# Performance work log

Measured on AMD Instinct MI355X. Metric: run time of the kernel, lower is better.

## Reference

```python
import jax, jax.numpy as jnp
import numpy as np

N = 100000        # nodes
E = 1600000       # edges (avg degree 16)
IN_C = 128
HID = 128
OUT_C = 18


def setup_inputs() -> dict:
    key = jax.random.key(0)
    k_x, k_e, k_w1, k_b1, k_w2, k_b2 = jax.random.split(key, 6)
    x = jax.random.normal(k_x, (N, IN_C), dtype=jnp.float32)
    edge_index = jax.random.randint(k_e, (2, E), 0, N, dtype=jnp.int64)
    # Glorot-ish init for linear weights, zero bias (PyG GCNConv defaults)
    W1 = jax.random.normal(k_w1, (IN_C, HID), dtype=jnp.float32) / np.sqrt(IN_C)
    b1 = jnp.zeros((HID,), dtype=jnp.float32)
    W2 = jax.random.normal(k_w2, (HID, OUT_C), dtype=jnp.float32) / np.sqrt(HID)
    b2 = jnp.zeros((OUT_C,), dtype=jnp.float32)
    return {"x": x, "edge_index": edge_index, "W1": W1, "b1": b1, "W2": W2, "b2": b2}


def _gcn_conv(x, src, dst, norm, W, b, n_nodes):
    # PyG GCNConv: linear transform, then normalized scatter-add aggregation
    h = x @ W                                   # [N, d_out]
    msg = h[src] * norm[:, None]                # gather + scale: [E+N, d_out]
    out = jax.ops.segment_sum(msg, dst, num_segments=n_nodes)
    return out + b


def reference(x, edge_index, W1, b1, W2, b2):
    src, dst = edge_index[0], edge_index[1]
    loop = jnp.arange(N, dtype=edge_index.dtype)
    src_f = jnp.concatenate([src, loop])        # add self-loops
    dst_f = jnp.concatenate([dst, loop])
    # symmetric normalization deg^-1/2[src] * deg^-1/2[dst] (with self-loops)
    deg = jax.ops.segment_sum(jnp.ones_like(dst_f, dtype=x.dtype), dst_f, num_segments=N)
    dinv = jnp.where(deg > 0, jax.lax.rsqrt(deg), 0.0)
    norm = dinv[src_f] * dinv[dst_f]            # [E+N]

    h = _gcn_conv(x, src_f, dst_f, norm, W1, b1, N)
    h = jax.nn.relu(h)
    # dropout is identity in eval mode (training=False)
    h = _gcn_conv(h, src_f, dst_f, norm, W2, b2, N)
    return jax.nn.log_softmax(h, axis=1)
```

## Files before the change

kernel.cpp:

```cpp
#include <hip/hip_runtime.h>
#include <math.h>

#define NN 100000
#define NE 1600000
#define CH  128
#define CO  18
#define NPB 256
#define NBUK ((NN + NPB - 1) / NPB)
#define EPB 4096
#define NBB ((NE + EPB - 1) / EPB)

typedef unsigned int uint;
typedef unsigned short ushort;
typedef float floatx4 __attribute__((ext_vector_type(4)));
typedef short short8 __attribute__((ext_vector_type(8)));
typedef ushort ushort4v __attribute__((ext_vector_type(4)));

__device__ __forceinline__ float bf_lo(uint u) { return __uint_as_float(u << 16); }
__device__ __forceinline__ float bf_hi(uint u) { return __uint_as_float(u & 0xFFFF0000u); }
__device__ __forceinline__ ushort f2bf(float f) {
    uint u = __float_as_uint(f);
    u += 0x7FFFu + ((u >> 16) & 1u);
    return (ushort)(u >> 16);
}
__device__ __forceinline__ uint pack_bf16(float a, float b) {
    return (uint)f2bf(a) | ((uint)f2bf(b) << 16);
}


union FatLDS {
    int h[NBUK];
    struct { ushort As[128 * 128]; ushort Bs[128 * 128]; } g;
};

__global__ __launch_bounds__(256, 2) void k_fat1(const int* __restrict__ dst,
                                                 int* __restrict__ bcnt,
                                                 const float* __restrict__ x,
                                                 const float* __restrict__ W1,
                                                 ushort* __restrict__ h1s) {
    __shared__ FatLDS L;
    int tid = threadIdx.x;

    if (blockIdx.x < NBB) {
        for (int i = tid; i < NBUK; i += 256) L.h[i] = 0;
        __syncthreads();
        int e0 = blockIdx.x * EPB;
#pragma unroll
        for (int i = 0; i < EPB / 256; ++i) {
            int e = e0 + i * 256 + tid;
            if (e < NE) atomicAdd(&L.h[dst[e] >> 8], 1);
        }
        __syncthreads();
        for (int i = tid; i < NBUK; i += 256)
            if (L.h[i]) atomicAdd(&bcnt[i], L.h[i]);
        return;
    }

    int row0 = (blockIdx.x - NBB) * 128;

    for (int p = tid; p < 8192; p += 256) {
        int kp = p >> 7, n = p & 127;
        float w0 = W1[(2 * kp) * 128 + n];
        float w1 = W1[(2 * kp + 1) * 128 + n];
        ((uint*)L.g.Bs)[(n * 64 + kp) ^ ((n & 7) << 2)] = pack_bf16(w0, w1);
    }
    for (int i = 0; i < 16; ++i) {
        int flat = i * 256 + tid;
        int r = flat >> 5, c4 = flat & 31;
        int gr = row0 + r;
        float4 v = (gr < NN) ? ((const float4*)x)[(size_t)gr * 32 + c4]
                             : make_float4(0.f, 0.f, 0.f, 0.f);
        ushort4v p;
        p.x = f2bf(v.x); p.y = f2bf(v.y); p.z = f2bf(v.z); p.w = f2bf(v.w);
        int idx = (r * 128 + c4 * 4) ^ ((r & 7) << 3);
        *(ushort4v*)&L.g.As[idx] = p;
    }
    __syncthreads();

    int lane = tid & 63;
    int wave = tid >> 6;
    int wrow = wave * 32;
    int lr = lane & 15;
    int lk8 = (lane >> 4) * 8;

    floatx4 acc[2][8];
#pragma unroll
    for (int a = 0; a < 2; ++a)
#pragma unroll
        for (int b = 0; b < 8; ++b) acc[a][b] = (floatx4)(0.0f);

#pragma unroll
    for (int ks = 0; ks < 4; ++ks) {
        int k0 = ks * 32 + lk8;
        int r0r = wrow + lr;
        int r1r = wrow + 16 + lr;
        short8 a0 = *(const short8*)&L.g.As[(r0r * 128 + k0) ^ ((r0r & 7) << 3)];
        short8 a1 = *(const short8*)&L.g.As[(r1r * 128 + k0) ^ ((r1r & 7) << 3)];
#pragma unroll
        for (int nt = 0; nt < 8; ++nt) {
            int n = nt * 16 + lr;
            short8 bf = *(const short8*)&L.g.Bs[(n * 128 + k0) ^ ((n & 7) << 3)];
            acc[0][nt] = __builtin_amdgcn_mfma_f32_16x16x32_bf16(a0, bf, acc[0][nt], 0, 0, 0);
            acc[1][nt] = __builtin_amdgcn_mfma_f32_16x16x32_bf16(a1, bf, acc[1][nt], 0, 0, 0);
        }
    }

    int drow = (lane >> 4) * 4;
#pragma unroll
    for (int rt = 0; rt < 2; ++rt) {
#pragma unroll
        for (int i = 0; i < 4; ++i) {
            int gr = row0 + wrow + rt * 16 + drow + i;
            if (gr < NN) {
                size_t base = (size_t)gr * 128;
#pragma unroll
                for (int nt = 0; nt < 8; ++nt)
                    h1s[base + nt * 16 + lr] = f2bf(acc[rt][nt][i]);
            }
        }
    }
}


__global__ __launch_bounds__(512) void k_bscan(const int* __restrict__ bcnt,
                                               int* __restrict__ bbase,
                                               int* __restrict__ bcur) {
    __shared__ int s[512];
    int tid = threadIdx.x;
    int c = (tid < NBUK) ? bcnt[tid] : 0;
    s[tid] = c;
    __syncthreads();
    for (int off = 1; off < 512; off <<= 1) {
        int t = (tid >= off) ? s[tid - off] : 0;
        __syncthreads();
        s[tid] += t;
        __syncthreads();
    }
    if (tid < NBUK) {
        int ex = s[tid] - c;
        bbase[tid] = ex;
        bcur[tid] = ex;
    }
    if (tid == NBUK) bbase[NBUK] = NE;
}

__global__ __launch_bounds__(256) void k_bin(const int* __restrict__ src,
                                             const int* __restrict__ dst,
                                             int* __restrict__ bcur,
                                             uint* __restrict__ etmp) {
    __shared__ int h[NBUK];
    __shared__ int base[NBUK];
    int tid = threadIdx.x;
    for (int i = tid; i < NBUK; i += 256) h[i] = 0;
    __syncthreads();

    int e0 = blockIdx.x * EPB;
    int sv[EPB / 256], dv[EPB / 256];
#pragma unroll
    for (int i = 0; i < EPB / 256; ++i) {
        int e = e0 + i * 256 + tid;
        if (e < NE) {
            sv[i] = src[e];
            dv[i] = dst[e];
            atomicAdd(&h[dv[i] >> 8], 1);
        } else {
            dv[i] = -1;
        }
    }
    __syncthreads();
    for (int i = tid; i < NBUK; i += 256)
        base[i] = h[i] ? atomicAdd(&bcur[i], h[i]) : 0;
    __syncthreads();
    for (int i = tid; i < NBUK; i += 256) h[i] = 0;
    __syncthreads();
#pragma unroll
    for (int i = 0; i < EPB / 256; ++i) {
        if (dv[i] >= 0) {
            int b = dv[i] >> 8;
            int pos = base[b] + atomicAdd(&h[b], 1);
            etmp[pos] = ((uint)sv[i] << 8) | ((uint)dv[i] & 255u);
        }
    }
}

__global__ __launch_bounds__(256) void k_pass2(const int* __restrict__ bbase,
                                               const uint* __restrict__ etmp,
                                               int* __restrict__ row_start,
                                               float* __restrict__ dinv,
                                               int* __restrict__ csr_src) {
    __shared__ int hist[NPB];
    __shared__ int s[NPB];
    __shared__ int cur[NPB];
    int tid = threadIdx.x;
    int b = blockIdx.x;
    int e0 = bbase[b], e1 = bbase[b + 1];

    hist[tid] = 0;
    __syncthreads();
    for (int e = e0 + tid; e < e1; e += 256)
        atomicAdd(&hist[etmp[e] & 255u], 1);
    __syncthreads();

    int c = hist[tid];
    s[tid] = c;
    __syncthreads();
    for (int off = 1; off < 256; off <<= 1) {
        int t = (tid >= off) ? s[tid - off] : 0;
        __syncthreads();
        s[tid] += t;
        __syncthreads();
    }
    int pfx = s[tid] - c;
    s[tid] = pfx;
    cur[tid] = 0;

    int node = b * NPB + tid;
    if (node < NN) {
        row_start[node] = e0 + pfx;
        dinv[node] = rsqrtf((float)c + 1.0f);
    }
    if (b == NBUK - 1 && tid == 0) row_start[NN] = NE;
    __syncthreads();

    for (int e = e0 + tid; e < e1; e += 256) {
        uint r = etmp[e];
        int n = (int)(r & 255u);
        int p = e0 + s[n] + atomicAdd(&cur[n], 1);
        csr_src[p] = (int)(r >> 8);
    }
}


__global__ __launch_bounds__(256) void k_agg1(const int* __restrict__ row_start,
                                              const int* __restrict__ csr_src,
                                              const float* __restrict__ dinv,
                                              const uint* __restrict__ h1u,
                                              const float* __restrict__ b1,
                                              uint* __restrict__ h1ru) {
    int wave = threadIdx.x >> 6;
    int lane = threadIdx.x & 63;
    int i = blockIdx.x * 4 + wave;
    if (i >= NN) return;
    int r0 = row_start[i], r1 = row_start[i + 1];
    float di = dinv[i];
    float ax = 0.0f, ay = 0.0f;

    int j = r0;
    for (; j + 7 < r1; j += 8) {
        int s0 = csr_src[j],     s1 = csr_src[j + 1];
        int s2 = csr_src[j + 2], s3 = csr_src[j + 3];
        int s4 = csr_src[j + 4], s5 = csr_src[j + 5];
        int s6 = csr_src[j + 6], s7 = csr_src[j + 7];
        float w0 = dinv[s0] * di, w1 = dinv[s1] * di;
        float w2 = dinv[s2] * di, w3 = dinv[s3] * di;
        float w4 = dinv[s4] * di, w5 = dinv[s5] * di;
        float w6 = dinv[s6] * di, w7 = dinv[s7] * di;
        uint u0 = h1u[(size_t)s0 * 64 + lane];
        uint u1 = h1u[(size_t)s1 * 64 + lane];
        uint u2 = h1u[(size_t)s2 * 64 + lane];
        uint u3 = h1u[(size_t)s3 * 64 + lane];
        uint u4 = h1u[(size_t)s4 * 64 + lane];
        uint u5 = h1u[(size_t)s5 * 64 + lane];
        uint u6 = h1u[(size_t)s6 * 64 + lane];
        uint u7 = h1u[(size_t)s7 * 64 + lane];
        ax += w0 * bf_lo(u0) + w1 * bf_lo(u1) + w2 * bf_lo(u2) + w3 * bf_lo(u3)
            + w4 * bf_lo(u4) + w5 * bf_lo(u5) + w6 * bf_lo(u6) + w7 * bf_lo(u7);
        ay += w0 * bf_hi(u0) + w1 * bf_hi(u1) + w2 * bf_hi(u2) + w3 * bf_hi(u3)
            + w4 * bf_hi(u4) + w5 * bf_hi(u5) + w6 * bf_hi(u6) + w7 * bf_hi(u7);
    }
    for (; j < r1; ++j) {
        int s0 = csr_src[j];
        float w0 = dinv[s0] * di;
        uint u0 = h1u[(size_t)s0 * 64 + lane];
        ax += w0 * bf_lo(u0);
        ay += w0 * bf_hi(u0);
    }

    uint us = h1u[(size_t)i * 64 + lane];
    float2 bb = ((const float2*)b1)[lane];
    float di2 = di * di;
    float ox = fmaxf(ax + di2 * bf_lo(us) + bb.x, 0.0f);
    float oy = fmaxf(ay + di2 * bf_hi(us) + bb.y, 0.0f);
    h1ru[(size_t)i * 64 + lane] = pack_bf16(ox, oy);
}


__global__ __launch_bounds__(256, 2) void k_gemm2(const uint* __restrict__ h1ru,
                                                  const float* __restrict__ W2,
                                                  ushort* __restrict__ h2b) {
    __shared__ float xs[128][129];
    __shared__ float Ws[128 * 18];
    int row0 = blockIdx.x * 128;
    int tid = threadIdx.x;

    for (int i = tid; i < 128 * 18; i += 256) Ws[i] = W2[i];
    for (int i = tid; i < 128 * 64; i += 256) {
        int r = i >> 6, c2 = i & 63;
        int gr = row0 + r;
        uint u = (gr < NN) ? h1ru[(size_t)gr * 64 + c2] : 0u;
        xs[r][2 * c2]     = bf_lo(u);
        xs[r][2 * c2 + 1] = bf_hi(u);
    }
    __syncthreads();

    int rl   = tid & 127;
    int half = tid >> 7;
    int j0   = half * 9;
    float acc[9];
#pragma unroll
    for (int j = 0; j < 9; ++j) acc[j] = 0.0f;

#pragma unroll 4
    for (int k = 0; k < 128; ++k) {
        float xv = xs[rl][k];
#pragma unroll
        for (int j = 0; j < 9; ++j)
            acc[j] += xv * Ws[k * 18 + j0 + j];
    }
    int gr = row0 + rl;
    if (gr < NN) {
#pragma unroll
        for (int j = 0; j < 9; ++j)
            h2b[(size_t)gr * 24 + j0 + j] = f2bf(acc[j]);
    }
}


__device__ __forceinline__ void acc_row(float* acc, float wgt,
                                        uint4 av, uint4 bv, uint cv) {
    acc[0]  += wgt * bf_lo(av.x); acc[1]  += wgt * bf_hi(av.x);
    acc[2]  += wgt * bf_lo(av.y); acc[3]  += wgt * bf_hi(av.y);
    acc[4]  += wgt * bf_lo(av.z); acc[5]  += wgt * bf_hi(av.z);
    acc[6]  += wgt * bf_lo(av.w); acc[7]  += wgt * bf_hi(av.w);
    acc[8]  += wgt * bf_lo(bv.x); acc[9]  += wgt * bf_hi(bv.x);
    acc[10] += wgt * bf_lo(bv.y); acc[11] += wgt * bf_hi(bv.y);
    acc[12] += wgt * bf_lo(bv.z); acc[13] += wgt * bf_hi(bv.z);
    acc[14] += wgt * bf_lo(bv.w); acc[15] += wgt * bf_hi(bv.w);
    acc[16] += wgt * bf_lo(cv);   acc[17] += wgt * bf_hi(cv);
}

__global__ __launch_bounds__(256) void k_agg2(const int* __restrict__ row_start,
                                              const int* __restrict__ csr_src,
                                              const float* __restrict__ dinv,
                                              const uint* __restrict__ h2u,
                                              const float* __restrict__ b2,
                                              float* __restrict__ out) {
    int i = blockIdx.x * 256 + threadIdx.x;
    if (i >= NN) return;
    int r0 = row_start[i], r1 = row_start[i + 1];
    float di = dinv[i];
    float acc[CO];
#pragma unroll
    for (int j = 0; j < CO; ++j) acc[j] = 0.0f;

    int e = r0;
    for (; e + 3 < r1; e += 4) {
        int s0 = csr_src[e],     s1 = csr_src[e + 1];
        int s2 = csr_src[e + 2], s3 = csr_src[e + 3];
        float w0 = dinv[s0] * di, w1 = dinv[s1] * di;
        float w2 = dinv[s2] * di, w3 = dinv[s3] * di;
        const uint* p0 = h2u + (size_t)s0 * 12;
        const uint* p1 = h2u + (size_t)s1 * 12;
        const uint* p2 = h2u + (size_t)s2 * 12;
        const uint* p3 = h2u + (size_t)s3 * 12;
        uint4 a0 = *(const uint4*)p0, b0 = *(const uint4*)(p0 + 4); uint c0 = p0[8];
        uint4 a1 = *(const uint4*)p1, b1v = *(const uint4*)(p1 + 4); uint c1 = p1[8];
        uint4 a2 = *(const uint4*)p2, b2v = *(const uint4*)(p2 + 4); uint c2 = p2[8];
        uint4 a3 = *(const uint4*)p3, b3v = *(const uint4*)(p3 + 4); uint c3 = p3[8];
        acc_row(acc, w0, a0, b0, c0);
        acc_row(acc, w1, a1, b1v, c1);
        acc_row(acc, w2, a2, b2v, c2);
        acc_row(acc, w3, a3, b3v, c3);
    }
    for (; e < r1; ++e) {
        int s = csr_src[e];
        float w = dinv[s] * di;
        const uint* p = h2u + (size_t)s * 12;
        uint4 a = *(const uint4*)p, b = *(const uint4*)(p + 4); uint c = p[8];
        acc_row(acc, w, a, b, c);
    }

    float di2 = di * di;
    const uint* pi = h2u + (size_t)i * 12;
    uint4 ia = *(const uint4*)pi, ib = *(const uint4*)(pi + 4); uint ic = pi[8];
    acc_row(acc, di2, ia, ib, ic);

    float m = -1e30f;
#pragma unroll
    for (int j = 0; j < CO; ++j) {
        acc[j] += b2[j];
        m = fmaxf(m, acc[j]);
    }
    float sum = 0.0f;
#pragma unroll
    for (int j = 0; j < CO; ++j) sum += expf(acc[j] - m);
    float lse = logf(sum);
    float* op = out + (size_t)i * CO;
#pragma unroll
    for (int j = 0; j < CO; ++j) op[j] = acc[j] - m - lse;
}


extern "C" void kernel_launch(void* const* d_in, const int* in_sizes, int n_in,
                              void* d_out, int out_size, void* d_ws, size_t ws_size,
                              hipStream_t stream) {
    const float* x  = (const float*)d_in[0];
    const int*   ei = (const int*)d_in[1];
    const float* W1 = (const float*)d_in[2];
    const float* b1 = (const float*)d_in[3];
    const float* W2 = (const float*)d_in[4];
    const float* b2 = (const float*)d_in[5];
    float* out = (float*)d_out;

    const int* src = ei;
    const int* dst = ei + NE;

    uint* h1u  = (uint*)d_ws;
    uint* h1ru = h1u + (size_t)NN * 64;
    uint* h2u  = h1ru + (size_t)NN * 64;
    float* dinv = (float*)(h2u + (size_t)NN * 12);
    int* row_start = (int*)(dinv + NN);
    int* csr_src   = row_start + NN + 1;
    uint* etmp     = (uint*)(csr_src + NE);
    int* bcnt      = (int*)(etmp + NE);
    int* bbase     = bcnt + NBUK;
    int* bcur      = bbase + NBUK + 1;

    hipMemsetAsync(bcnt, 0, NBUK * sizeof(int), stream);

    k_fat1<<<NBB + (NN + 127) / 128, 256, 0, stream>>>(dst, bcnt, x, W1, (ushort*)h1u);
    k_bscan<<<1, 512, 0, stream>>>(bcnt, bbase, bcur);
    k_bin<<<NBB, 256, 0, stream>>>(src, dst, bcur, etmp);
    k_pass2<<<NBUK, 256, 0, stream>>>(bbase, etmp, row_start, dinv, csr_src);

    k_agg1<<<(NN + 3) / 4, 256, 0, stream>>>(row_start, csr_src, dinv, h1u, b1, h1ru);
    k_gemm2<<<(NN + 127) / 128, 256, 0, stream>>>(h1ru, W2, (ushort*)h2u);
    k_agg2<<<(NN + 255) / 256, 256, 0, stream>>>(row_start, csr_src, dinv, h2u, b2, out);
}
```

Baseline: 249.0 us.

## Stage GEMM1 output through LDS, reuse bin ranks, split h2 layout

The first GEMM now writes its bf16 tile into shared memory and then stores it to global memory as coalesced 32-bit words, replacing scattered 16-bit stores. The binning kernel keeps the rank returned by the first shared atomic, which removes the histogram reset and the second atomic pass. The layer-2 features move from a padded 48-byte row to a 32-byte-aligned 16-column array plus a separate 2-column array, so the gather in aggregation 2 touches fewer bytes and aligned lines. The cost is an extra LDS round trip with two barriers in GEMM1, and a second scattered 4-byte load per edge in aggregation 2.

```diff
diff --git a/kernel.cpp b/kernel.cpp
--- a/kernel.cpp
+++ b/kernel.cpp
@@ -37,7 +37,7 @@
                                                  int* __restrict__ bcnt,
                                                  const float* __restrict__ x,
                                                  const float* __restrict__ W1,
-                                                 ushort* __restrict__ h1s) {
+                                                 uint* __restrict__ h1w) {
     __shared__ FatLDS L;
     int tid = threadIdx.x;
 
@@ -105,19 +105,23 @@
         }
     }
 
+    __syncthreads();
     int drow = (lane >> 4) * 4;
 #pragma unroll
     for (int rt = 0; rt < 2; ++rt) {
 #pragma unroll
         for (int i = 0; i < 4; ++i) {
-            int gr = row0 + wrow + rt * 16 + drow + i;
-            if (gr < NN) {
-                size_t base = (size_t)gr * 128;
-#pragma unroll
-                for (int nt = 0; nt < 8; ++nt)
-                    h1s[base + nt * 16 + lr] = f2bf(acc[rt][nt][i]);
-            }
-        }
+            int lrow = wrow + rt * 16 + drow + i;
+#pragma unroll
+            for (int nt = 0; nt < 8; ++nt)
+                L.g.As[lrow * 128 + nt * 16 + lr] = f2bf(acc[rt][nt][i]);
+        }
+    }
+    __syncthreads();
+    for (int p = tid; p < 8192; p += 256) {
+        int r = p >> 6;
+        int gr = row0 + r;
+        if (gr < NN) h1w[(size_t)gr * 64 + (p & 63)] = ((const uint*)L.g.As)[p];
     }
 }
 
@@ -155,14 +159,14 @@
     __syncthreads();
 
     int e0 = blockIdx.x * EPB;
-    int sv[EPB / 256], dv[EPB / 256];
+    int sv[EPB / 256], dv[EPB / 256], rk[EPB / 256];
 #pragma unroll
     for (int i = 0; i < EPB / 256; ++i) {
         int e = e0 + i * 256 + tid;
         if (e < NE) {
             sv[i] = src[e];
             dv[i] = dst[e];
-            atomicAdd(&h[dv[i] >> 8], 1);
+            rk[i] = atomicAdd(&h[dv[i] >> 8], 1);
         } else {
             dv[i] = -1;
         }
@@ -170,15 +174,12 @@
     __syncthreads();
     for (int i = tid; i < NBUK; i += 256)
         base[i] = h[i] ? atomicAdd(&bcur[i], h[i]) : 0;
-    __syncthreads();
-    for (int i = tid; i < NBUK; i += 256) h[i] = 0;
     __syncthreads();
 #pragma unroll
     for (int i = 0; i < EPB / 256; ++i) {
         if (dv[i] >= 0) {
             int b = dv[i] >> 8;
-            int pos = base[b] + atomicAdd(&h[b], 1);
-            etmp[pos] = ((uint)sv[i] << 8) | ((uint)dv[i] & 255u);
+            etmp[base[b] + rk[i]] = ((uint)sv[i] << 8) | ((uint)dv[i] & 255u);
         }
     }
 }
@@ -287,7 +288,8 @@
 
 __global__ __launch_bounds__(256, 2) void k_gemm2(const uint* __restrict__ h1ru,
                                                   const float* __restrict__ W2,
-                                                  ushort* __restrict__ h2b) {
+                                                  ushort* __restrict__ h2a,
+                                                  ushort* __restrict__ h2c) {
     __shared__ float xs[128][129];
     __shared__ float Ws[128 * 18];
     int row0 = blockIdx.x * 128;
@@ -320,8 +322,12 @@
     int gr = row0 + rl;
     if (gr < NN) {
 #pragma unroll
-        for (int j = 0; j < 9; ++j)
-            h2b[(size_t)gr * 24 + j0 + j] = f2bf(acc[j]);
+        for (int j = 0; j < 9; ++j) {
+            int col = j0 + j;
+            ushort v = f2bf(acc[j]);
+            if (col < 16) h2a[(size_t)gr * 16 + col] = v;
+            else          h2c[(size_t)gr * 2 + (col - 16)] = v;
+        }
     }
 }
 
@@ -342,7 +348,8 @@
 __global__ __launch_bounds__(256) void k_agg2(const int* __restrict__ row_start,
                                               const int* __restrict__ csr_src,
                                               const float* __restrict__ dinv,
-                                              const uint* __restrict__ h2u,
+                                              const uint* __restrict__ h2a,
+                                              const uint* __restrict__ h2c,
                                               const float* __restrict__ b2,
                                               float* __restrict__ out) {
     int i = blockIdx.x * 256 + threadIdx.x;
@@ -359,14 +366,14 @@
         int s2 = csr_src[e + 2], s3 = csr_src[e + 3];
         float w0 = dinv[s0] * di, w1 = dinv[s1] * di;
         float w2 = dinv[s2] * di, w3 = dinv[s3] * di;
-        const uint* p0 = h2u + (size_t)s0 * 12;
-        const uint* p1 = h2u + (size_t)s1 * 12;
-        const uint* p2 = h2u + (size_t)s2 * 12;
-        const uint* p3 = h2u + (size_t)s3 * 12;
-        uint4 a0 = *(const uint4*)p0, b0 = *(const uint4*)(p0 + 4); uint c0 = p0[8];
-        uint4 a1 = *(const uint4*)p1, b1v = *(const uint4*)(p1 + 4); uint c1 = p1[8];
-        uint4 a2 = *(const uint4*)p2, b2v = *(const uint4*)(p2 + 4); uint c2 = p2[8];
-        uint4 a3 = *(const uint4*)p3, b3v = *(const uint4*)(p3 + 4); uint c3 = p3[8];
+        const uint4* p0 = (const uint4*)(h2a + (size_t)s0 * 8);
+        const uint4* p1 = (const uint4*)(h2a + (size_t)s1 * 8);
+        const uint4* p2 = (const uint4*)(h2a + (size_t)s2 * 8);
+        const uint4* p3 = (const uint4*)(h2a + (size_t)s3 * 8);
+        uint4 a0 = p0[0], b0 = p0[1]; uint c0 = h2c[s0];
+        uint4 a1 = p1[0], b1v = p1[1]; uint c1 = h2c[s1];
+        uint4 a2 = p2[0], b2v = p2[1]; uint c2 = h2c[s2];
+        uint4 a3 = p3[0], b3v = p3[1]; uint c3 = h2c[s3];
         acc_row(acc, w0, a0, b0, c0);
         acc_row(acc, w1, a1, b1v, c1);
         acc_row(acc, w2, a2, b2v, c2);
@@ -375,14 +382,14 @@
     for (; e < r1; ++e) {
         int s = csr_src[e];
         float w = dinv[s] * di;
-        const uint* p = h2u + (size_t)s * 12;
-        uint4 a = *(const uint4*)p, b = *(const uint4*)(p + 4); uint c = p[8];
+        const uint4* p = (const uint4*)(h2a + (size_t)s * 8);
+        uint4 a = p[0], b = p[1]; uint c = h2c[s];
         acc_row(acc, w, a, b, c);
     }
 
     float di2 = di * di;
-    const uint* pi = h2u + (size_t)i * 12;
-    uint4 ia = *(const uint4*)pi, ib = *(const uint4*)(pi + 4); uint ic = pi[8];
+    const uint4* pi = (const uint4*)(h2a + (size_t)i * 8);
+    uint4 ia = pi[0], ib = pi[1]; uint ic = h2c[i];
     acc_row(acc, di2, ia, ib, ic);
 
     float m = -1e30f;
@@ -417,8 +424,9 @@
 
     uint* h1u  = (uint*)d_ws;
     uint* h1ru = h1u + (size_t)NN * 64;
-    uint* h2u  = h1ru + (size_t)NN * 64;
-    float* dinv = (float*)(h2u + (size_t)NN * 12);
+    uint* h2a  = h1ru + (size_t)NN * 64;
+    uint* h2c  = h2a + (size_t)NN * 8;
+    float* dinv = (float*)(h2c + NN);
     int* row_start = (int*)(dinv + NN);
     int* csr_src   = row_start + NN + 1;
     uint* etmp     = (uint*)(csr_src + NE);
@@ -428,12 +436,12 @@
 
     hipMemsetAsync(bcnt, 0, NBUK * sizeof(int), stream);
 
-    k_fat1<<<NBB + (NN + 127) / 128, 256, 0, stream>>>(dst, bcnt, x, W1, (ushort*)h1u);
+    k_fat1<<<NBB + (NN + 127) / 128, 256, 0, stream>>>(dst, bcnt, x, W1, h1u);
     k_bscan<<<1, 512, 0, stream>>>(bcnt, bbase, bcur);
     k_bin<<<NBB, 256, 0, stream>>>(src, dst, bcur, etmp);
     k_pass2<<<NBUK, 256, 0, stream>>>(bbase, etmp, row_start, dinv, csr_src);
 
     k_agg1<<<(NN + 3) / 4, 256, 0, stream>>>(row_start, csr_src, dinv, h1u, b1, h1ru);
-    k_gemm2<<<(NN + 127) / 128, 256, 0, stream>>>(h1ru, W2, (ushort*)h2u);
-    k_agg2<<<(NN + 255) / 256, 256, 0, stream>>>(row_start, csr_src, dinv, h2u, b2, out);
-}
+    k_gemm2<<<(NN + 127) / 128, 256, 0, stream>>>(h1ru, W2, (ushort*)h2a, (ushort*)h2c);
+    k_agg2<<<(NN + 255) / 256, 256, 0, stream>>>(row_start, csr_src, dinv, h2a, h2c, b2, out);
+}
```

Result: slower. 254.9 us (+2.4%).

## Slice h1 into 16-column panels and aggregate each slice separately

Applied to the files above, without the earlier changes.

The first GEMM now writes h1 as eight column-slabs of 16 bf16 values (32 bytes per node), stored slab-major. The aggregation kernel assigns each block to one slab, so the gathered working set per slab (about 3.2 MB) can stay cache-resident, and each wave handles 8 edges at once with 8 lanes per edge, reduced by shuffles. In exchange, csr_src, dinv and row_start are re-read eight times, each gather moves only 32 bytes, and the output write covers only a 32-byte piece of each row.

```diff
diff --git a/kernel.cpp b/kernel.cpp
--- a/kernel.cpp
+++ b/kernel.cpp
@@ -9,6 +9,7 @@
 #define NBUK ((NN + NPB - 1) / NPB)
 #define EPB 4096
 #define NBB ((NE + EPB - 1) / EPB)
+#define NG  3125
 
 typedef unsigned int uint;
 typedef unsigned short ushort;
@@ -37,7 +38,7 @@
                                                  int* __restrict__ bcnt,
                                                  const float* __restrict__ x,
                                                  const float* __restrict__ W1,
-                                                 ushort* __restrict__ h1s) {
+                                                 ushort* __restrict__ h1sl) {
     __shared__ FatLDS L;
     int tid = threadIdx.x;
 
@@ -112,10 +113,9 @@
         for (int i = 0; i < 4; ++i) {
             int gr = row0 + wrow + rt * 16 + drow + i;
             if (gr < NN) {
-                size_t base = (size_t)gr * 128;
 #pragma unroll
                 for (int nt = 0; nt < 8; ++nt)
-                    h1s[base + nt * 16 + lr] = f2bf(acc[rt][nt][i]);
+                    h1sl[((size_t)nt * NN + gr) * 16 + lr] = f2bf(acc[rt][nt][i]);
             }
         }
     }
@@ -234,54 +234,44 @@
 __global__ __launch_bounds__(256) void k_agg1(const int* __restrict__ row_start,
                                               const int* __restrict__ csr_src,
                                               const float* __restrict__ dinv,
-                                              const uint* __restrict__ h1u,
+                                              const uint* __restrict__ h1sl,
                                               const float* __restrict__ b1,
                                               uint* __restrict__ h1ru) {
+    int s = blockIdx.x & 7;
+    int g = blockIdx.x >> 3;
     int wave = threadIdx.x >> 6;
     int lane = threadIdx.x & 63;
-    int i = blockIdx.x * 4 + wave;
-    if (i >= NN) return;
-    int r0 = row_start[i], r1 = row_start[i + 1];
-    float di = dinv[i];
-    float ax = 0.0f, ay = 0.0f;
-
-    int j = r0;
-    for (; j + 7 < r1; j += 8) {
-        int s0 = csr_src[j],     s1 = csr_src[j + 1];
-        int s2 = csr_src[j + 2], s3 = csr_src[j + 3];
-        int s4 = csr_src[j + 4], s5 = csr_src[j + 5];
-        int s6 = csr_src[j + 6], s7 = csr_src[j + 7];
-        float w0 = dinv[s0] * di, w1 = dinv[s1] * di;
-        float w2 = dinv[s2] * di, w3 = dinv[s3] * di;
-        float w4 = dinv[s4] * di, w5 = dinv[s5] * di;
-        float w6 = dinv[s6] * di, w7 = dinv[s7] * di;
-        uint u0 = h1u[(size_t)s0 * 64 + lane];
-        uint u1 = h1u[(size_t)s1 * 64 + lane];
-        uint u2 = h1u[(size_t)s2 * 64 + lane];
-        uint u3 = h1u[(size_t)s3 * 64 + lane];
-        uint u4 = h1u[(size_t)s4 * 64 + lane];
-        uint u5 = h1u[(size_t)s5 * 64 + lane];
-        uint u6 = h1u[(size_t)s6 * 64 + lane];
-        uint u7 = h1u[(size_t)s7 * 64 + lane];
-        ax += w0 * bf_lo(u0) + w1 * bf_lo(u1) + w2 * bf_lo(u2) + w3 * bf_lo(u3)
-            + w4 * bf_lo(u4) + w5 * bf_lo(u5) + w6 * bf_lo(u6) + w7 * bf_lo(u7);
-        ay += w0 * bf_hi(u0) + w1 * bf_hi(u1) + w2 * bf_hi(u2) + w3 * bf_hi(u3)
-            + w4 * bf_hi(u4) + w5 * bf_hi(u5) + w6 * bf_hi(u6) + w7 * bf_hi(u7);
-    }
-    for (; j < r1; ++j) {
-        int s0 = csr_src[j];
-        float w0 = dinv[s0] * di;
-        uint u0 = h1u[(size_t)s0 * 64 + lane];
-        ax += w0 * bf_lo(u0);
-        ay += w0 * bf_hi(u0);
-    }
-
-    uint us = h1u[(size_t)i * 64 + lane];
-    float2 bb = ((const float2*)b1)[lane];
-    float di2 = di * di;
-    float ox = fmaxf(ax + di2 * bf_lo(us) + bb.x, 0.0f);
-    float oy = fmaxf(ay + di2 * bf_hi(us) + bb.y, 0.0f);
-    h1ru[(size_t)i * 64 + lane] = pack_bf16(ox, oy);
+    int es = lane >> 3;
+    int u  = lane & 7;
+    const uint* tab = h1sl + (size_t)s * NN * 8;
+
+    for (int i = g * 4 + wave; i < NN; i += NG * 4) {
+        int r0 = row_start[i], r1 = row_start[i + 1];
+        float di = dinv[i];
+        float ax = 0.0f, ay = 0.0f;
+        for (int jb = r0; jb < r1; jb += 16) {
+            int j1 = jb + es, j2 = jb + 8 + es;
+            int s1 = csr_src[j1 < r1 ? j1 : r0];
+            int s2 = csr_src[j2 < r1 ? j2 : r0];
+            float w1 = (j1 < r1) ? dinv[s1] * di : 0.0f;
+            float w2 = (j2 < r1) ? dinv[s2] * di : 0.0f;
+            uint v1 = tab[(size_t)s1 * 8 + u];
+            uint v2 = tab[(size_t)s2 * 8 + u];
+            ax += w1 * bf_lo(v1) + w2 * bf_lo(v2);
+            ay += w1 * bf_hi(v1) + w2 * bf_hi(v2);
+        }
+        ax += __shfl_xor(ax, 8);  ay += __shfl_xor(ay, 8);
+        ax += __shfl_xor(ax, 16); ay += __shfl_xor(ay, 16);
+        ax += __shfl_xor(ax, 32); ay += __shfl_xor(ay, 32);
+        if (es == 0) {
+            uint us = tab[(size_t)i * 8 + u];
+            float2 bb = ((const float2*)b1)[s * 8 + u];
+            float di2 = di * di;
+            float ox = fmaxf(ax + di2 * bf_lo(us) + bb.x, 0.0f);
+            float oy = fmaxf(ay + di2 * bf_hi(us) + bb.y, 0.0f);
+            h1ru[(size_t)i * 64 + s * 8 + u] = pack_bf16(ox, oy);
+        }
+    }
 }
 
 
@@ -433,7 +423,7 @@
     k_bin<<<NBB, 256, 0, stream>>>(src, dst, bcur, etmp);
     k_pass2<<<NBUK, 256, 0, stream>>>(bbase, etmp, row_start, dinv, csr_src);
 
-    k_agg1<<<(NN + 3) / 4, 256, 0, stream>>>(row_start, csr_src, dinv, h1u, b1, h1ru);
+    k_agg1<<<NG * 8, 256, 0, stream>>>(row_start, csr_src, dinv, h1u, b1, h1ru);
     k_gemm2<<<(NN + 127) / 128, 256, 0, stream>>>(h1ru, W2, (ushort*)h2u);
     k_agg2<<<(NN + 255) / 256, 256, 0, stream>>>(row_start, csr_src, dinv, h2u, b2, out);
 }
```

After: 414.7 us. +66.5%, slower.
